# Kernel tuning notes

Measured on AMD Instinct MI355X. Metric: run time of the kernel, lower is better.

The kernel has to match this reference:

```python
import jax, jax.numpy as jnp
import numpy as np

B, C1, C2, H, W = 16, 64, 64, 160, 160
K, KS, HID = 4, 3, 16  # K kernels, 3x3, hidden = max(int(64/16),16)=16
EPS = 1e-5


def setup_inputs() -> dict:
    key = jax.random.key(0)
    ks = jax.random.split(key, 8)
    fan_out = KS * KS * C2
    return {
        "x": jax.random.normal(ks[0], (B, C1, H, W), jnp.float32),
        # K candidate conv kernels and biases
        "Wk": jax.random.normal(ks[1], (K, C2, C1, KS, KS), jnp.float32) * np.sqrt(2.0 / fan_out),
        "bk": jnp.zeros((K, C2), jnp.float32),
        # attention trunk: 1x1 conv C1->HID (no bias), BN, ReLU
        "Wfc": jax.random.normal(ks[2], (HID, C1), jnp.float32) * 0.1,
        "gamma_h": jnp.ones((HID,), jnp.float32),
        "beta_h": jnp.zeros((HID,), jnp.float32),
        # four attention heads
        "Wf": jax.random.normal(ks[3], (C2, HID), jnp.float32) * 0.1,
        "bf": jnp.zeros((C2,), jnp.float32),
        "Ws": jax.random.normal(ks[4], (KS * KS, HID), jnp.float32) * 0.1,
        "bs": jnp.zeros((KS * KS,), jnp.float32),
        "Wc": jax.random.normal(ks[5], (C1, HID), jnp.float32) * 0.1,
        "bc": jnp.zeros((C1,), jnp.float32),
        "Ww": jax.random.normal(ks[6], (K, HID), jnp.float32) * 0.1,
        "bw": jnp.zeros((K,), jnp.float32),
        # outer BatchNorm2d params
        "gamma_o": jnp.ones((C2,), jnp.float32),
        "beta_o": jnp.zeros((C2,), jnp.float32),
    }


def reference(x, Wk, bk, Wfc, gamma_h, beta_h, Wf, bf, Ws, bs, Wc, bc, Ww, bw, gamma_o, beta_o):
    # ---- per-sample attention over K kernels ----
    ctx = x.mean(axis=(2, 3))                      # (B, C1)  global avg pool
    h = ctx @ Wfc.T                                # (B, HID) 1x1 conv == linear
    mu = h.mean(axis=0)
    var = h.var(axis=0)                            # biased, as torch BN training
    h = (h - mu) / jnp.sqrt(var + EPS) * gamma_h + beta_h
    h = jax.nn.relu(h)
    attn_f = jax.nn.sigmoid(h @ Wf.T + bf)         # (B, C2)
    attn_s = jax.nn.sigmoid(h @ Ws.T + bs).reshape(B, KS, KS)
    attn_c = jax.nn.sigmoid(h @ Wc.T + bc)         # (B, C1)
    attn_w = jax.nn.softmax(h @ Ww.T + bw, axis=-1)  # (B, K)

    # attn: (B, K, C2, C1, KS, KS) via broadcasting
    attn = (attn_w[:, :, None, None, None, None]
            * attn_f[:, None, :, None, None, None]
            * attn_c[:, None, None, :, None, None]
            * attn_s[:, None, None, None, :, :])
    weight = jnp.sum(attn * Wk[None], axis=1)      # (B, C2, C1, KS, KS)
    bias = attn_w @ bk                             # (B, C2)

    # ---- batched conv as grouped conv with groups=B ----
    out = jax.lax.conv_general_dilated(
        x.reshape(1, B * C1, H, W),
        weight.reshape(B * C2, C1, KS, KS),
        window_strides=(1, 1), padding=((1, 1), (1, 1)),
        dimension_numbers=('NCHW', 'OIHW', 'NCHW'),
        feature_group_count=B)                     # (1, B*C2, H, W)
    out = out.reshape(B, C2, H, W) + bias[:, :, None, None]

    # ---- outer BatchNorm2d (training stats) + SiLU ----
    mu_o = out.mean(axis=(0, 2, 3))
    var_o = out.var(axis=(0, 2, 3))
    out = (out - mu_o[None, :, None, None]) / jnp.sqrt(var_o + EPS)[None, :, None, None]
    out = out * gamma_o[None, :, None, None] + beta_o[None, :, None, None]
    return out * jax.nn.sigmoid(out)               # SiLU
```

## Files before the change

kernel.cpp:

```cpp
#include <hip/hip_runtime.h>
#include <math.h>

#define BB 16
#define C1 64
#define C2 64
#define HH 160
#define WW 160
#define KK 4
#define HID 16
#define EPS 1e-5f
#define HWSZ (HH*WW)
#define NPB (BB*HWSZ)

#define WS_AF    1024
#define WS_AC    2048
#define WS_AS    3072
#define WS_AW    3216
#define WS_BIAS  3280
#define WS_SC    4304
#define WS_SH    4368
#define WS_STATS 4432
#define NSLOT    32
#define WS_PART  8704
#define WS_ZERO  49664
#define WS_WEFF  50944
#define WS_XBF   345856

typedef __attribute__((ext_vector_type(8)))  short bf16x8;
typedef __attribute__((ext_vector_type(16))) float f32x16;

__device__ __forceinline__ unsigned short f2bf(float f) {
    unsigned int u = __float_as_uint(f);
    unsigned int r = (u + 0x7FFFu + ((u >> 16) & 1u)) >> 16;
    return (unsigned short)r;
}

__device__ __forceinline__ void gload16(const void* g, void* l) {
    __builtin_amdgcn_global_load_lds(
        (const __attribute__((address_space(1))) unsigned int*)g,
        (__attribute__((address_space(3))) unsigned int*)l, 16, 0, 0);
}

__global__ __launch_bounds__(256) void xprep_kernel(const float* __restrict__ x,
                                                    float* __restrict__ ws) {
    __shared__ float lds[10240];
    int bcc = blockIdx.y;
    int rg = blockIdx.x;
    int t = threadIdx.x;

    const float* src = x + (size_t)bcc * 16 * HWSZ + (size_t)rg * 4 * WW;
    float4* l4 = (float4*)lds;
    #pragma unroll
    for (int i = 0; i < 10; ++i) {
        int g = i * 256 + t;
        int ch = g / 160, rem = g - ch * 160;
        l4[g] = *(const float4*)(src + (size_t)ch * HWSZ + rem * 4);
    }
    __syncthreads();

    {
        int ch = t >> 4, j = t & 15;
        float s = 0.f;
        #pragma unroll
        for (int m = 0; m < 40; ++m) s += lds[ch * 640 + j + 16 * m];
        #pragma unroll
        for (int o = 8; o > 0; o >>= 1) s += __shfl_down(s, o, 16);
        if (j == 0) ws[WS_PART + ((size_t)bcc * 40 + rg) * 16 + ch] = s;
    }

    uint4* dst = (uint4*)(ws + WS_XBF) + ((size_t)bcc * 160 + rg * 4) * 320;
    #pragma unroll
    for (int i = 0; i < 5; ++i) {
        int u = i * 256 + t;
        int row = u / 320, rem = u - row * 320;
        int col = rem >> 1, p = rem & 1;
        int h = p ^ ((col >> 2) & 1) ^ 1;
        union { uint4 q; unsigned short us[8]; } pk;
        #pragma unroll
        for (int k = 0; k < 8; ++k)
            pk.us[k] = f2bf(lds[(h * 8 + k) * 640 + row * 160 + col]);
        dst[u] = pk.q;
    }
}

__global__ void attn_kernel(float* __restrict__ ws,
    const float* __restrict__ Wfc, const float* __restrict__ gh, const float* __restrict__ bh,
    const float* __restrict__ Wf,  const float* __restrict__ bf,
    const float* __restrict__ Wsm, const float* __restrict__ bs,
    const float* __restrict__ Wc,  const float* __restrict__ bc,
    const float* __restrict__ Ww,  const float* __restrict__ bw,
    const float* __restrict__ bk) {
    __shared__ float ctxs[16][64];
    __shared__ float hs[16][16];
    __shared__ float aw[16][4];
    int t = threadIdx.x;

    #pragma unroll
    for (int q = 0; q < 4; ++q) {
        int idx = t * 4 + q;
        int b = idx >> 6, c1 = idx & 63;
        const float* pp = ws + WS_PART + ((size_t)(b * 4 + (c1 >> 4)) * 40) * 16 + (c1 & 15);
        float s = 0.f;
        #pragma unroll
        for (int rg = 0; rg < 40; ++rg) s += pp[rg * 16];
        ctxs[b][c1] = s * (1.0f / (float)HWSZ);
    }
    __syncthreads();
    {
        int b = t >> 4, j = t & 15;
        const float* wr = Wfc + j * 64;
        float s = 0.f;
        #pragma unroll
        for (int c = 0; c < 64; c++) s += ctxs[b][c] * wr[c];
        hs[b][j] = s;
    }
    __syncthreads();
    if (t < 16) {
        int j = t;
        float mu = 0.f;
        #pragma unroll
        for (int b = 0; b < 16; b++) mu += hs[b][j];
        mu *= (1.f / 16.f);
        float vr = 0.f;
        #pragma unroll
        for (int b = 0; b < 16; b++) { float d = hs[b][j] - mu; vr += d * d; }
        vr *= (1.f / 16.f);
        float sc = gh[j] * rsqrtf(vr + EPS);
        float sh = bh[j] - mu * sc;
        #pragma unroll
        for (int b = 0; b < 16; b++) {
            float v = hs[b][j] * sc + sh;
            hs[b][j] = v > 0.f ? v : 0.f;
        }
    }
    __syncthreads();
    if (t < 16) {
        int b = t;
        float l[4]; float mx = -1e30f;
        #pragma unroll
        for (int k = 0; k < 4; k++) {
            float s = bw[k];
            #pragma unroll
            for (int j = 0; j < 16; j++) s += hs[b][j] * Ww[k * 16 + j];
            l[k] = s; mx = fmaxf(mx, s);
        }
        float den = 0.f;
        #pragma unroll
        for (int k = 0; k < 4; k++) { l[k] = expf(l[k] - mx); den += l[k]; }
        float r = 1.f / den;
        #pragma unroll
        for (int k = 0; k < 4; k++) { float v = l[k] * r; aw[b][k] = v; ws[WS_AW + b * 4 + k] = v; }
    }
    #pragma unroll
    for (int q = 0; q < 4; q++) {
        int idx = t * 4 + q;
        int b = idx >> 6, c2 = idx & 63;
        float sf = bf[c2], sc2 = bc[c2];
        #pragma unroll
        for (int j = 0; j < 16; j++) {
            float hv = hs[b][j];
            sf  += hv * Wf[c2 * 16 + j];
            sc2 += hv * Wc[c2 * 16 + j];
        }
        ws[WS_AF + idx] = 1.f / (1.f + expf(-sf));
        ws[WS_AC + idx] = 1.f / (1.f + expf(-sc2));
    }
    if (t < 144) {
        int b = t / 9, uv = t % 9;
        float s = bs[uv];
        #pragma unroll
        for (int j = 0; j < 16; j++) s += hs[b][j] * Wsm[uv * 16 + j];
        ws[WS_AS + t] = 1.f / (1.f + expf(-s));
    }
    __syncthreads();
    #pragma unroll
    for (int q = 0; q < 4; q++) {
        int idx = t * 4 + q;
        int b = idx >> 6, c2 = idx & 63;
        float s = 0.f;
        #pragma unroll
        for (int k = 0; k < 4; k++) s += aw[b][k] * bk[k * 64 + c2];
        ws[WS_BIAS + idx] = s;
    }
    for (int i = t; i < NSLOT * 128; i += 256) ws[WS_STATS + i] = 0.f;
    for (int i = t; i < 1280; i += 256) ws[WS_ZERO + i] = 0.f;
}

__global__ void wprep_kernel(const float* __restrict__ Wk, float* __restrict__ ws) {
    int b = blockIdx.y;
    int tid = blockIdx.x * 256 + threadIdx.x;
    int h = tid & 1;
    int c2 = (tid >> 1) & 63;
    int g = tid >> 7;
    int uv = g % 9;
    int chunk = g / 9;
    const float* awp = ws + WS_AW + b * 4;
    float aw0 = awp[0], aw1 = awp[1], aw2 = awp[2], aw3 = awp[3];
    float af = ws[WS_AF + b * 64 + c2];
    float as_ = ws[WS_AS + b * 9 + uv];
    union { uint4 q; unsigned short u[8]; } pk;
    #pragma unroll
    for (int j = 0; j < 8; ++j) {
        int c1 = chunk * 16 + h * 8 + j;
        const float* wp = Wk + (size_t)(c2 * 64 + c1) * 9 + uv;
        float s = aw0 * wp[0] + aw1 * wp[64 * 64 * 9] + aw2 * wp[2 * 64 * 64 * 9] + aw3 * wp[3 * 64 * 64 * 9];
        float w = s * af * ws[WS_AC + b * 64 + c1] * as_;
        pk.u[j] = f2bf(w);
    }
    int unit = ((chunk * 9 + uv) * 64 + c2) * 2 + (h ^ ((c2 >> 2) & 1));
    ((uint4*)(ws + WS_WEFF))[(size_t)b * 4608 + unit] = pk.q;
}

__launch_bounds__(256, 2)
__global__ void conv_kernel(const float* __restrict__ wsf, float* __restrict__ out) {
    __shared__ uint4 xs[6 * 162 * 2];
    __shared__ uint4 wsh[1152];
    __shared__ float bsh[64];
    __shared__ float sst[128];

    int id = blockIdx.x;
    int b = id & 15;
    int bx = id >> 4;
    int y0 = bx * 4;
    int t = threadIdx.x;
    int wv = t >> 6;
    int lane = t & 63;
    int l31 = lane & 31;
    int l5 = lane >> 5;

    if (t < 64) bsh[t] = wsf[WS_BIAS + b * 64 + t];
    if (t >= 64 && t < 192) sst[t - 64] = 0.f;
    if (t >= 192 && t < 216) {
        int q = t - 192;
        int r = q >> 2, side = (q >> 1) & 1, p = q & 1;
        xs[(r * 162 + side * 161) * 2 + p] = make_uint4(0, 0, 0, 0);
    }
    int rbad = (bx == 0) ? 0 : (bx == 39 ? 5 : -1);
    if (rbad >= 0) {
        for (int i = t; i < 320; i += 256)
            xs[(rbad * 162 + 1) * 2 + i] = make_uint4(0, 0, 0, 0);
    }

    const uint4* weff = (const uint4*)(wsf + WS_WEFF) + (size_t)b * 4608;
    const uint4* xbf  = (const uint4*)(wsf + WS_XBF);

    f32x16 acc[2][5];
    #pragma unroll
    for (int a = 0; a < 2; ++a)
        #pragma unroll
        for (int j = 0; j < 5; ++j)
            #pragma unroll
            for (int r = 0; r < 16; ++r) acc[a][j][r] = 0.f;

    int svz[3];
    #pragma unroll
    for (int v = 0; v < 3; ++v) svz[v] = l5 ^ (((l31 + v + 3) >> 2) & 1);
    int awz = l5 ^ ((l31 >> 2) & 1);

    for (int cc = 0; cc < 4; ++cc) {
        __syncthreads();
        for (int i = wv; i < 18; i += 4)
            gload16(weff + (size_t)cc * 1152 + i * 64 + lane, (char*)wsh + i * 1024);
        for (int i = wv; i < 30; i += 4) {
            int r = i / 5, seg = i % 5;
            int gy = y0 - 1 + r;
            if (gy >= 0 && gy < HH)
                gload16(xbf + (((size_t)b * 4 + cc) * 160 + gy) * 320 + seg * 64 + lane,
                        (char*)xs + ((r * 162 + 1) * 2 + seg * 64) * 16);
        }
        __syncthreads();

        #pragma unroll
        for (int u = 0; u < 3; ++u) {
            #pragma unroll
            for (int v = 0; v < 3; ++v) {
                int uv = u * 3 + v;
                const uint4* ap = &wsh[(uv * 64 + l31) * 2 + awz];
                bf16x8 a0 = *(bf16x8*)ap;
                bf16x8 a1 = *(bf16x8*)(ap + 64);
                const uint4* bp = &xs[((wv + u) * 162 + l31 + v) * 2 + svz[v]];
                #pragma unroll
                for (int j = 0; j < 5; ++j) {
                    bf16x8 bb = *(bf16x8*)(bp + j * 64);
                    acc[0][j] = __builtin_amdgcn_mfma_f32_32x32x16_bf16(a0, bb, acc[0][j], 0, 0, 0);
                    acc[1][j] = __builtin_amdgcn_mfma_f32_32x32x16_bf16(a1, bb, acc[1][j], 0, 0, 0);
                }
            }
        }
    }

    float* outb = out + (size_t)b * C2 * HWSZ + (size_t)(y0 + wv) * WW;
    #pragma unroll
    for (int a = 0; a < 2; ++a) {
        int cb = a * 32 + 4 * l5;
        float sr[16], qr[16];
        #pragma unroll
        for (int r = 0; r < 16; ++r) {
            int c2r = cb + (r & 3) + 8 * (r >> 2);
            float bias = bsh[c2r];
            float s = 0.f, q = 0.f;
            #pragma unroll
            for (int j = 0; j < 5; ++j) {
                float v = acc[a][j][r] + bias;
                outb[(size_t)c2r * HWSZ + j * 32 + l31] = v;
                s += v;
                q = fmaf(v, v, q);
            }
            sr[r] = s; qr[r] = q;
        }
        #pragma unroll
        for (int k = 0; k < 4; ++k) {
            int m = 1 << k, n = 8 >> k;
            #pragma unroll
            for (int i = 0; i < 8; ++i) {
                if (i < n) {
                    float ks = (l31 & m) ? sr[i + n] : sr[i];
                    float ss = (l31 & m) ? sr[i] : sr[i + n];
                    sr[i] = ks + __shfl_xor(ss, m, 64);
                    float kq = (l31 & m) ? qr[i + n] : qr[i];
                    float sq = (l31 & m) ? qr[i] : qr[i + n];
                    qr[i] = kq + __shfl_xor(sq, m, 64);
                }
            }
        }
        sr[0] += __shfl_xor(sr[0], 16, 64);
        qr[0] += __shfl_xor(qr[0], 16, 64);
        if (l31 < 16) {
            int rf = ((l31 & 1) << 3) | ((l31 & 2) << 1) | ((l31 & 4) >> 1) | ((l31 & 8) >> 3);
            int c2r = cb + (rf & 3) + 8 * (rf >> 2);
            atomicAdd(&sst[c2r], sr[0]);
            atomicAdd(&sst[64 + c2r], qr[0]);
        }
    }
    __syncthreads();
    if (t < 128) {
        int slot = id & (NSLOT - 1);
        atomicAdd((float*)wsf + WS_STATS + slot * 128 + t, sst[t]);
    }
}

__global__ void bnstat_kernel(float* __restrict__ ws, const float* __restrict__ go,
                              const float* __restrict__ bo) {
    int c = threadIdx.x;
    float s = 0.f, q = 0.f;
    for (int sl = 0; sl < NSLOT; sl++) {
        s += ws[WS_STATS + sl * 128 + c];
        q += ws[WS_STATS + sl * 128 + 64 + c];
    }
    float mu  = s * (1.0f / (float)NPB);
    float var = q * (1.0f / (float)NPB) - mu * mu;
    float sc  = go[c] * rsqrtf(var + EPS);
    ws[WS_SC + c] = sc;
    ws[WS_SH + c] = bo[c] - mu * sc;
}

__global__ void bnact_kernel(float* __restrict__ out, const float* __restrict__ ws) {
    __shared__ float sc[64], sh[64];
    if (threadIdx.x < 64) {
        sc[threadIdx.x] = ws[WS_SC + threadIdx.x];
        sh[threadIdx.x] = ws[WS_SH + threadIdx.x];
    }
    __syncthreads();
    const int n4 = BB * C2 * HWSZ / 4;
    for (int i = blockIdx.x * blockDim.x + threadIdx.x; i < n4; i += gridDim.x * blockDim.x) {
        float4 v = ((float4*)out)[i];
        int c = ((i * 4) / HWSZ) & 63;
        float s = sc[c], h = sh[c];
        v.x = v.x * s + h; v.y = v.y * s + h; v.z = v.z * s + h; v.w = v.w * s + h;
        v.x = v.x / (1.f + __expf(-v.x));
        v.y = v.y / (1.f + __expf(-v.y));
        v.z = v.z / (1.f + __expf(-v.z));
        v.w = v.w / (1.f + __expf(-v.w));
        ((float4*)out)[i] = v;
    }
}

extern "C" void kernel_launch(void* const* d_in, const int* in_sizes, int n_in,
                              void* d_out, int out_size, void* d_ws, size_t ws_size,
                              hipStream_t stream) {
    const float* x   = (const float*)d_in[0];
    const float* Wk  = (const float*)d_in[1];
    const float* bk  = (const float*)d_in[2];
    const float* Wfc = (const float*)d_in[3];
    const float* gh  = (const float*)d_in[4];
    const float* bh  = (const float*)d_in[5];
    const float* Wf  = (const float*)d_in[6];
    const float* bf  = (const float*)d_in[7];
    const float* Wsm = (const float*)d_in[8];
    const float* bs  = (const float*)d_in[9];
    const float* Wc  = (const float*)d_in[10];
    const float* bc  = (const float*)d_in[11];
    const float* Ww  = (const float*)d_in[12];
    const float* bw  = (const float*)d_in[13];
    const float* go  = (const float*)d_in[14];
    const float* bo  = (const float*)d_in[15];
    float* out = (float*)d_out;
    float* ws  = (float*)d_ws;

    xprep_kernel<<<dim3(40, 64), dim3(256), 0, stream>>>(x, ws);
    attn_kernel<<<dim3(1), dim3(256), 0, stream>>>(ws, Wfc, gh, bh, Wf, bf, Wsm, bs, Wc, bc, Ww, bw, bk);
    wprep_kernel<<<dim3(18, 16), dim3(256), 0, stream>>>(Wk, ws);
    conv_kernel<<<dim3(640), dim3(256), 0, stream>>>(ws, out);
    bnstat_kernel<<<dim3(1), dim3(64), 0, stream>>>(ws, go, bo);
    bnact_kernel<<<dim3(2048), dim3(256), 0, stream>>>(out, ws);
}
```

Measured before the change: 133.4 us.

## Halve conv block to two output rows with 128 threads and regroup stat reduction

The conv kernel now uses 128-thread blocks, each covering 2 output rows instead of 4, launched as 1280 blocks instead of 640. The halo tile shrinks to 4 rows and each wave loads fixed slices with unrolled loops. The epilogue reduces per-channel statistics in two groups of 8 registers instead of 16, which lowers register pressure. The cost is more redundant halo loads and a full weight-tile reload per block, since each block reuses the weights across fewer rows, plus twice as many global stat atomics.

```diff
diff --git a/kernel.cpp b/kernel.cpp
--- a/kernel.cpp
+++ b/kernel.cpp
@@ -211,9 +211,9 @@
     ((uint4*)(ws + WS_WEFF))[(size_t)b * 4608 + unit] = pk.q;
 }
 
-__launch_bounds__(256, 2)
+__launch_bounds__(128, 2)
 __global__ void conv_kernel(const float* __restrict__ wsf, float* __restrict__ out) {
-    __shared__ uint4 xs[6 * 162 * 2];
+    __shared__ uint4 xs[4 * 162 * 2];
     __shared__ uint4 wsh[1152];
     __shared__ float bsh[64];
     __shared__ float sst[128];
@@ -221,7 +221,7 @@
     int id = blockIdx.x;
     int b = id & 15;
     int bx = id >> 4;
-    int y0 = bx * 4;
+    int y0 = bx * 2;
     int t = threadIdx.x;
     int wv = t >> 6;
     int lane = t & 63;
@@ -229,15 +229,17 @@
     int l5 = lane >> 5;
 
     if (t < 64) bsh[t] = wsf[WS_BIAS + b * 64 + t];
-    if (t >= 64 && t < 192) sst[t - 64] = 0.f;
-    if (t >= 192 && t < 216) {
-        int q = t - 192;
+    if (t >= 64 && t < 80) {
+        int q = t - 64;
         int r = q >> 2, side = (q >> 1) & 1, p = q & 1;
         xs[(r * 162 + side * 161) * 2 + p] = make_uint4(0, 0, 0, 0);
     }
-    int rbad = (bx == 0) ? 0 : (bx == 39 ? 5 : -1);
+    {
+        sst[t] = 0.f;
+    }
+    int rbad = (bx == 0) ? 0 : (bx == 79 ? 3 : -1);
     if (rbad >= 0) {
-        for (int i = t; i < 320; i += 256)
+        for (int i = t; i < 320; i += 128)
             xs[(rbad * 162 + 1) * 2 + i] = make_uint4(0, 0, 0, 0);
     }
 
@@ -252,21 +254,24 @@
             #pragma unroll
             for (int r = 0; r < 16; ++r) acc[a][j][r] = 0.f;
 
-    int svz[3];
-    #pragma unroll
-    for (int v = 0; v < 3; ++v) svz[v] = l5 ^ (((l31 + v + 3) >> 2) & 1);
-    int awz = l5 ^ ((l31 >> 2) & 1);
-
     for (int cc = 0; cc < 4; ++cc) {
         __syncthreads();
-        for (int i = wv; i < 18; i += 4)
+        #pragma unroll
+        for (int k = 0; k < 9; ++k) {
+            int i = wv * 9 + k;
             gload16(weff + (size_t)cc * 1152 + i * 64 + lane, (char*)wsh + i * 1024);
-        for (int i = wv; i < 30; i += 4) {
-            int r = i / 5, seg = i % 5;
+        }
+        #pragma unroll
+        for (int rr = 0; rr < 2; ++rr) {
+            int r = wv * 2 + rr;
             int gy = y0 - 1 + r;
-            if (gy >= 0 && gy < HH)
-                gload16(xbf + (((size_t)b * 4 + cc) * 160 + gy) * 320 + seg * 64 + lane,
-                        (char*)xs + ((r * 162 + 1) * 2 + seg * 64) * 16);
+            if (gy >= 0 && gy < HH) {
+                const uint4* src = xbf + (((size_t)b * 4 + cc) * 160 + gy) * 320 + lane;
+                char* dstb = (char*)xs + ((r * 162 + 1) * 2) * 16;
+                #pragma unroll
+                for (int seg = 0; seg < 5; ++seg)
+                    gload16(src + seg * 64, dstb + seg * 1024);
+            }
         }
         __syncthreads();
 
@@ -275,10 +280,11 @@
             #pragma unroll
             for (int v = 0; v < 3; ++v) {
                 int uv = u * 3 + v;
-                const uint4* ap = &wsh[(uv * 64 + l31) * 2 + awz];
+                const uint4* ap = &wsh[(uv * 64 + l31) * 2 + (l5 ^ ((l31 >> 2) & 1))];
                 bf16x8 a0 = *(bf16x8*)ap;
                 bf16x8 a1 = *(bf16x8*)(ap + 64);
-                const uint4* bp = &xs[((wv + u) * 162 + l31 + v) * 2 + svz[v]];
+                const uint4* bp = &xs[((wv + u) * 162 + l31 + v) * 2 +
+                                      (l5 ^ (((l31 + v + 3) >> 2) & 1))];
                 #pragma unroll
                 for (int j = 0; j < 5; ++j) {
                     bf16x8 bb = *(bf16x8*)(bp + j * 64);
@@ -293,47 +299,54 @@
     #pragma unroll
     for (int a = 0; a < 2; ++a) {
         int cb = a * 32 + 4 * l5;
-        float sr[16], qr[16];
-        #pragma unroll
-        for (int r = 0; r < 16; ++r) {
-            int c2r = cb + (r & 3) + 8 * (r >> 2);
-            float bias = bsh[c2r];
-            float s = 0.f, q = 0.f;
+        #pragma unroll
+        for (int g = 0; g < 2; ++g) {
+            float sr[8], qr[8];
             #pragma unroll
-            for (int j = 0; j < 5; ++j) {
-                float v = acc[a][j][r] + bias;
-                outb[(size_t)c2r * HWSZ + j * 32 + l31] = v;
-                s += v;
-                q = fmaf(v, v, q);
+            for (int m = 0; m < 8; ++m) {
+                int r = g * 8 + m;
+                int c2r = cb + (r & 3) + 8 * (r >> 2);
+                float bias = bsh[c2r];
+                float s = 0.f, q = 0.f;
+                #pragma unroll
+                for (int j = 0; j < 5; ++j) {
+                    float v = acc[a][j][r] + bias;
+                    outb[(size_t)c2r * HWSZ + j * 32 + l31] = v;
+                    s += v;
+                    q = fmaf(v, v, q);
+                }
+                sr[m] = s; qr[m] = q;
             }
-            sr[r] = s; qr[r] = q;
-        }
-        #pragma unroll
-        for (int k = 0; k < 4; ++k) {
-            int m = 1 << k, n = 8 >> k;
             #pragma unroll
-            for (int i = 0; i < 8; ++i) {
-                if (i < n) {
-                    float ks = (l31 & m) ? sr[i + n] : sr[i];
-                    float ss = (l31 & m) ? sr[i] : sr[i + n];
-                    sr[i] = ks + __shfl_xor(ss, m, 64);
-                    float kq = (l31 & m) ? qr[i + n] : qr[i];
-                    float sq = (l31 & m) ? qr[i] : qr[i + n];
-                    qr[i] = kq + __shfl_xor(sq, m, 64);
+            for (int k = 0; k < 3; ++k) {
+                int mm = 1 << k, n = 4 >> k;
+                #pragma unroll
+                for (int i = 0; i < 4; ++i) {
+                    if (i < n) {
+                        float ks = (l31 & mm) ? sr[i + n] : sr[i];
+                        float ss = (l31 & mm) ? sr[i] : sr[i + n];
+                        sr[i] = ks + __shfl_xor(ss, mm, 64);
+                        float kq = (l31 & mm) ? qr[i + n] : qr[i];
+                        float sq = (l31 & mm) ? qr[i] : qr[i + n];
+                        qr[i] = kq + __shfl_xor(sq, mm, 64);
+                    }
                 }
             }
-        }
-        sr[0] += __shfl_xor(sr[0], 16, 64);
-        qr[0] += __shfl_xor(qr[0], 16, 64);
-        if (l31 < 16) {
-            int rf = ((l31 & 1) << 3) | ((l31 & 2) << 1) | ((l31 & 4) >> 1) | ((l31 & 8) >> 3);
-            int c2r = cb + (rf & 3) + 8 * (rf >> 2);
-            atomicAdd(&sst[c2r], sr[0]);
-            atomicAdd(&sst[64 + c2r], qr[0]);
-        }
-    }
-    __syncthreads();
-    if (t < 128) {
+            sr[0] += __shfl_xor(sr[0], 8, 64);
+            qr[0] += __shfl_xor(qr[0], 8, 64);
+            sr[0] += __shfl_xor(sr[0], 16, 64);
+            qr[0] += __shfl_xor(qr[0], 16, 64);
+            if (l31 < 8) {
+                int relem = ((l31 & 1) << 2) | (l31 & 2) | ((l31 & 4) >> 2);
+                int r = g * 8 + relem;
+                int c2r = cb + (r & 3) + 8 * (r >> 2);
+                atomicAdd(&sst[c2r], sr[0]);
+                atomicAdd(&sst[64 + c2r], qr[0]);
+            }
+        }
+    }
+    __syncthreads();
+    {
         int slot = id & (NSLOT - 1);
         atomicAdd((float*)wsf + WS_STATS + slot * 128 + t, sst[t]);
     }
@@ -400,7 +413,7 @@
     xprep_kernel<<<dim3(40, 64), dim3(256), 0, stream>>>(x, ws);
     attn_kernel<<<dim3(1), dim3(256), 0, stream>>>(ws, Wfc, gh, bh, Wf, bf, Wsm, bs, Wc, bc, Ww, bw, bk);
     wprep_kernel<<<dim3(18, 16), dim3(256), 0, stream>>>(Wk, ws);
-    conv_kernel<<<dim3(640), dim3(256), 0, stream>>>(ws, out);
+    conv_kernel<<<dim3(1280), dim3(128), 0, stream>>>(ws, out);
     bnstat_kernel<<<dim3(1), dim3(64), 0, stream>>>(ws, go, bo);
     bnact_kernel<<<dim3(2048), dim3(256), 0, stream>>>(out, ws);
 }
```

After: 132.4 us. Within noise of the previous version (-0.8%).
